# Kernel tuning notes

Measured on AMD Instinct MI355X. Metric: run time of the kernel, lower is better.

## Reference

```python
import jax, jax.numpy as jnp
import numpy as np

D_MODEL = 2048
N_HEADS = 16
HEAD_DIM = D_MODEL // N_HEADS  # 128
ROPE_THETA = 10000.0
BATCH = 2
SEQ_LEN = 2048  # == window_size -> dense causal SDPA path


def setup_inputs() -> dict:
    key = jax.random.key(0)
    ks = jax.random.split(key, 5)
    scale = 1.0 / np.sqrt(D_MODEL)
    x = jax.random.normal(ks[0], (BATCH, SEQ_LEN, D_MODEL), dtype=jnp.float32)
    # torch nn.Linear weights are stored (out_features, in_features); y = x @ W.T
    Wq = jax.random.normal(ks[1], (D_MODEL, D_MODEL), dtype=jnp.float32) * scale
    Wk = jax.random.normal(ks[2], (D_MODEL, D_MODEL), dtype=jnp.float32) * scale
    Wv = jax.random.normal(ks[3], (D_MODEL, D_MODEL), dtype=jnp.float32) * scale
    Wo = jax.random.normal(ks[4], (D_MODEL, D_MODEL), dtype=jnp.float32) * scale
    return {"x": x, "Wq": Wq, "Wk": Wk, "Wv": Wv, "Wo": Wo}


def _apply_rope(x):
    # x: [B, H, S, HEAD_DIM]; interleaved-pair RoPE, positions 0..S-1
    S = x.shape[2]
    inv_freq = 1.0 / (ROPE_THETA ** (jnp.arange(0, HEAD_DIM, 2, dtype=jnp.float32) / HEAD_DIM))
    t = jnp.arange(S, dtype=jnp.float32)
    freqs = jnp.outer(t, inv_freq)            # [S, HEAD_DIM//2]
    cos = jnp.cos(freqs)
    sin = jnp.sin(freqs)
    x1 = x[..., 0::2]
    x2 = x[..., 1::2]
    rot = jnp.stack([x1 * cos - x2 * sin, x1 * sin + x2 * cos], axis=-1)  # [B,H,S,hd/2,2]
    return rot.reshape(x.shape)


def reference(x, Wq, Wk, Wv, Wo):
    B, S, _ = x.shape
    q = (x @ Wq.T).reshape(B, S, N_HEADS, HEAD_DIM).transpose(0, 2, 1, 3)  # [B,H,S,D]
    k = (x @ Wk.T).reshape(B, S, N_HEADS, HEAD_DIM).transpose(0, 2, 1, 3)
    v = (x @ Wv.T).reshape(B, S, N_HEADS, HEAD_DIM).transpose(0, 2, 1, 3)
    q = _apply_rope(q)
    k = _apply_rope(k)
    scores = jnp.einsum("bhqd,bhkd->bhqk", q, k) / np.sqrt(HEAD_DIM).astype(np.float32)
    causal = jnp.tril(jnp.ones((S, S), dtype=bool))
    scores = jnp.where(causal, scores, -jnp.inf)
    attn = jax.nn.softmax(scores, axis=-1)
    out = jnp.einsum("bhqk,bhkd->bhqd", attn, v)
    out = out.transpose(0, 2, 1, 3).reshape(B, S, N_HEADS * HEAD_DIM)
    return out @ Wo.T
```

## Files before the change

### kernel.cpp

```cpp
#include <hip/hip_runtime.h>
#include <stdint.h>

#define D_MODEL 2048
#define SEQ     2048
#define BATCH   2
#define NHEAD   16
#define HD      128
#define MROWS   (BATCH*SEQ)

typedef short short8 __attribute__((ext_vector_type(8)));
typedef float f32x4  __attribute__((ext_vector_type(4)));

__device__ __forceinline__ unsigned short f2b(float f) {
  unsigned int u = __float_as_uint(f);
  u += 0x7fffu + ((u >> 16) & 1u);
  return (unsigned short)(u >> 16);
}
__device__ __forceinline__ float b2f(unsigned short s) {
  return __uint_as_float(((unsigned int)s) << 16);
}
__device__ __forceinline__ void gll16(const void* g, void* l) {
  __builtin_amdgcn_global_load_lds((const __attribute__((address_space(1))) void*)g,
                                   (__attribute__((address_space(3))) void*)l, 16, 0, 0);
}
__device__ __forceinline__ void barrier_nodrain() {
  asm volatile("" ::: "memory");
  __builtin_amdgcn_s_barrier();
  asm volatile("" ::: "memory");
}
template<int N> __device__ __forceinline__ void vmwait() {
  if constexpr (N == 0)       asm volatile("s_waitcnt vmcnt(0)" ::: "memory");
  else if constexpr (N == 1)  asm volatile("s_waitcnt vmcnt(1)" ::: "memory");
  else if constexpr (N == 2)  asm volatile("s_waitcnt vmcnt(2)" ::: "memory");
  else if constexpr (N == 3)  asm volatile("s_waitcnt vmcnt(3)" ::: "memory");
  else if constexpr (N == 4)  asm volatile("s_waitcnt vmcnt(4)" ::: "memory");
  else if constexpr (N == 5)  asm volatile("s_waitcnt vmcnt(5)" ::: "memory");
  else if constexpr (N == 6)  asm volatile("s_waitcnt vmcnt(6)" ::: "memory");
  else if constexpr (N == 7)  asm volatile("s_waitcnt vmcnt(7)" ::: "memory");
  else if constexpr (N == 8)  asm volatile("s_waitcnt vmcnt(8)" ::: "memory");
  else if constexpr (N == 10) asm volatile("s_waitcnt vmcnt(10)" ::: "memory");
  else                        asm volatile("s_waitcnt vmcnt(12)" ::: "memory");
}

__global__ __launch_bounds__(256) void cast_all(
    const float* __restrict__ x,  const float* __restrict__ Wq,
    const float* __restrict__ Wk, const float* __restrict__ Wv,
    const float* __restrict__ Wo, unsigned short* __restrict__ dst)
{
  size_t e = ((size_t)blockIdx.x * 256 + threadIdx.x) * 4;
  const size_t XN = (size_t)MROWS * D_MODEL;
  const size_t WN = (size_t)D_MODEL * D_MODEL;
  const float* src; size_t off;
  if (e < XN) { src = x; off = e; }
  else {
    size_t e2 = e - XN;
    int w = (int)(e2 >> 22);
    off = e2 & (WN - 1);
    src = (w == 0) ? Wq : (w == 1) ? Wk : (w == 2) ? Wv : Wo;
  }
  float4 v = *(const float4*)(src + off);
  ushort4 o;
  o.x = f2b(v.x); o.y = f2b(v.y); o.z = f2b(v.z); o.w = f2b(v.w);
  *(ushort4*)(dst + e) = o;
}

template<int BM, int LA>
__device__ __forceinline__ void gemm_2mp(
    const unsigned short* __restrict__ A, const unsigned short* __restrict__ Bw,
    unsigned short* __restrict__ As, unsigned short* __restrict__ Bs,
    int m0, int n0, int tid, f32x4 (&acc)[BM / 32][4])
{
  constexpr int K = D_MODEL, NT = K / 64;
  constexpr int HA = BM / 2;
  constexpr int MI = BM / 32, MIH = MI / 2;
  constexpr int AHALF = HA * 64;
  constexpr int BHALF = 128 * 64;
  constexpr int W1 = 2 * LA + 2;
  constexpr int W2 = 2 * LA + 4;
  const int wave = tid >> 6, lane = tid & 63, l15 = lane & 15, quad = lane >> 4;
  const int wr = wave >> 2, wc = wave & 3;
  const int rA = wr * 16 + l15;
  const int rB = wc * 16 + l15;
  const int swk = l15 & 7;

  auto stA = [&](int buf, int h, int t) {
    #pragma unroll
    for (int i = 0; i < LA; ++i) {
      int slot = i * 512 + tid, rw = slot >> 3, ch = slot & 7;
      gll16(A + (size_t)(m0 + h * HA + rw) * K + t * 64 + ((ch ^ (rw & 7)) * 8),
            As + (buf * 2 + h) * AHALF + (i * 512 + wave * 64) * 8);
    }
  };
  auto stB = [&](int buf, int h, int t) {
    #pragma unroll
    for (int i = 0; i < 2; ++i) {
      int slot = i * 512 + tid, rw = slot >> 3, ch = slot & 7;
      gll16(Bw + (size_t)(n0 + h * 128 + rw) * K + t * 64 + ((ch ^ (rw & 7)) * 8),
            Bs + (buf * 2 + h) * BHALF + (i * 512 + wave * 64) * 8);
    }
  };
  auto ldA = [&](int buf, int h, int ml, int ks) -> short8 {
    int rw = ml * 32 + rA;
    return *(const short8*)(As + (buf * 2 + h) * AHALF + rw * 64 + (((ks * 4 + quad) ^ swk) * 8));
  };
  auto ldB = [&](int buf, int h, int nl, int ks) -> short8 {
    int rw = nl * 64 + rB;
    return *(const short8*)(Bs + (buf * 2 + h) * BHALF + rw * 64 + (((ks * 4 + quad) ^ swk) * 8));
  };

  stA(0, 0, 0); stB(0, 1, 0);
  stB(0, 0, 0); stA(0, 1, 0);
  stA(1, 0, 1); stB(1, 1, 1);

  short8 ah[MIH][2], b0[2][2], b1[2][2];

  #pragma unroll 1
  for (int t = 0; t < NT; ++t) {
    const int buf = t & 1;

    if (t == NT - 1) vmwait<LA>(); else vmwait<W1>();
    barrier_nodrain();
    #pragma unroll
    for (int ml = 0; ml < MIH; ++ml) {
      ah[ml][0] = ldA(buf, 0, ml, 0); ah[ml][1] = ldA(buf, 0, ml, 1);
    }
    #pragma unroll
    for (int nl = 0; nl < 2; ++nl) {
      b0[nl][0] = ldB(buf, 0, nl, 0); b0[nl][1] = ldB(buf, 0, nl, 1);
      b1[nl][0] = ldB(buf, 1, nl, 0); b1[nl][1] = ldB(buf, 1, nl, 1);
    }
    if (t + 1 < NT) { stB(buf ^ 1, 0, t + 1); stA(buf ^ 1, 1, t + 1); }
    asm volatile("s_waitcnt lgkmcnt(0)" ::: "memory");
    __builtin_amdgcn_sched_barrier(0);
    __builtin_amdgcn_s_setprio(1);
    #pragma unroll
    for (int ml = 0; ml < MIH; ++ml)
      #pragma unroll
      for (int nl = 0; nl < 2; ++nl)
        #pragma unroll
        for (int ks = 0; ks < 2; ++ks)
          acc[ml][nl] = __builtin_amdgcn_mfma_f32_16x16x32_bf16(ah[ml][ks], b0[nl][ks], acc[ml][nl], 0, 0, 0);
    #pragma unroll
    for (int ml = 0; ml < MIH; ++ml)
      #pragma unroll
      for (int nl = 0; nl < 2; ++nl)
        #pragma unroll
        for (int ks = 0; ks < 2; ++ks)
          acc[ml][2 + nl] = __builtin_amdgcn_mfma_f32_16x16x32_bf16(ah[ml][ks], b1[nl][ks], acc[ml][2 + nl], 0, 0, 0);
    __builtin_amdgcn_s_setprio(0);

    if (t == NT - 1) vmwait<0>(); else vmwait<W2>();
    barrier_nodrain();
    #pragma unroll
    for (int ml = 0; ml < MIH; ++ml) {
      ah[ml][0] = ldA(buf, 1, ml, 0); ah[ml][1] = ldA(buf, 1, ml, 1);
    }
    if (t + 2 < NT) { stA(buf, 0, t + 2); stB(buf, 1, t + 2); }
    asm volatile("s_waitcnt lgkmcnt(0)" ::: "memory");
    __builtin_amdgcn_sched_barrier(0);
    __builtin_amdgcn_s_setprio(1);
    #pragma unroll
    for (int ml = 0; ml < MIH; ++ml)
      #pragma unroll
      for (int nl = 0; nl < 2; ++nl)
        #pragma unroll
        for (int ks = 0; ks < 2; ++ks)
          acc[MIH + ml][2 + nl] = __builtin_amdgcn_mfma_f32_16x16x32_bf16(ah[ml][ks], b1[nl][ks], acc[MIH + ml][2 + nl], 0, 0, 0);
    #pragma unroll
    for (int ml = 0; ml < MIH; ++ml)
      #pragma unroll
      for (int nl = 0; nl < 2; ++nl)
        #pragma unroll
        for (int ks = 0; ks < 2; ++ks)
          acc[MIH + ml][nl] = __builtin_amdgcn_mfma_f32_16x16x32_bf16(ah[ml][ks], b0[nl][ks], acc[MIH + ml][nl], 0, 0, 0);
    __builtin_amdgcn_s_setprio(0);
  }
}

template<int BM, int BN>
__device__ __forceinline__ void gemm_pipe(
    const unsigned short* __restrict__ A, const unsigned short* __restrict__ Bw,
    unsigned short* __restrict__ As, unsigned short* __restrict__ Bs,
    int m0, int n0, int tid, f32x4 (&acc)[BM / 32][4])
{
  constexpr int K  = D_MODEL;
  constexpr int NT = K / 64;
  constexpr int LA = BM / 64, LB = BN / 64;
  constexpr int LT = LA + LB;
  constexpr int MI = BM / 32, MH = MI / 2;
  const int wave = tid >> 6, lane = tid & 63, l15 = lane & 15, quad = lane >> 4;
  const int wr = wave >> 2, wc = wave & 3;
  const int sw = l15 & 7;
  const int arow = wr * (BM / 2) + l15;
  const int brow = wc * (BN / 4) + l15;

  auto stage = [&](int buf, int t) {
    const int kt = t * 64;
    #pragma unroll
    for (int i = 0; i < LA; ++i) {
      int slot = i * 512 + tid;
      int row = slot >> 3, ch = slot & 7;
      gll16(A + (size_t)(m0 + row) * K + kt + ((ch ^ (row & 7)) * 8),
            As + (size_t)buf * (BM * 64) + (size_t)(i * 512 + wave * 64) * 8);
    }
    #pragma unroll
    for (int i = 0; i < LB; ++i) {
      int slot = i * 512 + tid;
      int row = slot >> 3, ch = slot & 7;
      gll16(Bw + (size_t)(n0 + row) * K + kt + ((ch ^ (row & 7)) * 8),
            Bs + (size_t)buf * (BN * 64) + (size_t)(i * 512 + wave * 64) * 8);
    }
  };

  stage(0, 0);
  stage(1, 1);

  short8 ah[MH][2], bf[4][2];

  #pragma unroll 1
  for (int t = 0; t < NT; ++t) {
    const int cur = t & 1;
    if (t < NT - 1) {
      if constexpr (LT == 8) vmwait<8>(); else vmwait<6>();
    } else {
      vmwait<0>();
    }
    barrier_nodrain();

    const unsigned short* as = As + cur * (BM * 64);
    const unsigned short* bs = Bs + cur * (BN * 64);

    #pragma unroll
    for (int mi = 0; mi < MH; ++mi)
      #pragma unroll
      for (int ks = 0; ks < 2; ++ks)
        ah[mi][ks] = *(const short8*)(as + (arow + mi * 16) * 64 + (((ks * 4 + quad) ^ sw) * 8));
    #pragma unroll
    for (int ni = 0; ni < 2; ++ni)
      #pragma unroll
      for (int ks = 0; ks < 2; ++ks)
        bf[ni][ks] = *(const short8*)(bs + (brow + ni * 16) * 64 + (((ks * 4 + quad) ^ sw) * 8));
    __builtin_amdgcn_s_setprio(1);
    #pragma unroll
    for (int mi = 0; mi < MH; ++mi)
      #pragma unroll
      for (int ni = 0; ni < 2; ++ni)
        #pragma unroll
        for (int ks = 0; ks < 2; ++ks)
          acc[mi][ni] = __builtin_amdgcn_mfma_f32_16x16x32_bf16(ah[mi][ks], bf[ni][ks], acc[mi][ni], 0, 0, 0);
    __builtin_amdgcn_s_setprio(0);

    #pragma unroll
    for (int ni = 2; ni < 4; ++ni)
      #pragma unroll
      for (int ks = 0; ks < 2; ++ks)
        bf[ni][ks] = *(const short8*)(bs + (brow + ni * 16) * 64 + (((ks * 4 + quad) ^ sw) * 8));
    __builtin_amdgcn_s_setprio(1);
    #pragma unroll
    for (int mi = 0; mi < MH; ++mi)
      #pragma unroll
      for (int ni = 2; ni < 4; ++ni)
        #pragma unroll
        for (int ks = 0; ks < 2; ++ks)
          acc[mi][ni] = __builtin_amdgcn_mfma_f32_16x16x32_bf16(ah[mi][ks], bf[ni][ks], acc[mi][ni], 0, 0, 0);
    __builtin_amdgcn_s_setprio(0);

    #pragma unroll
    for (int mi = 0; mi < MH; ++mi)
      #pragma unroll
      for (int ks = 0; ks < 2; ++ks)
        ah[mi][ks] = *(const short8*)(as + (arow + (mi + MH) * 16) * 64 + (((ks * 4 + quad) ^ sw) * 8));
    __builtin_amdgcn_s_setprio(1);
    #pragma unroll
    for (int mi = 0; mi < MH; ++mi)
      #pragma unroll
      for (int ni = 2; ni < 4; ++ni)
        #pragma unroll
        for (int ks = 0; ks < 2; ++ks)
          acc[mi + MH][ni] = __builtin_amdgcn_mfma_f32_16x16x32_bf16(ah[mi][ks], bf[ni][ks], acc[mi + MH][ni], 0, 0, 0);
    #pragma unroll
    for (int mi = 0; mi < MH; ++mi)
      #pragma unroll
      for (int ni = 0; ni < 2; ++ni)
        #pragma unroll
        for (int ks = 0; ks < 2; ++ks)
          acc[mi + MH][ni] = __builtin_amdgcn_mfma_f32_16x16x32_bf16(ah[mi][ks], bf[ni][ks], acc[mi + MH][ni], 0, 0, 0);
    __builtin_amdgcn_s_setprio(0);

    barrier_nodrain();
    if (t + 2 < NT) stage(cur, t + 2);
  }
}

__global__ __launch_bounds__(512, 2) void gemm_qkv3(
    const unsigned short* __restrict__ Axb, const unsigned short* __restrict__ Wqkv,
    unsigned short* __restrict__ Qh, unsigned short* __restrict__ Kh,
    unsigned short* __restrict__ Vt)
{
  __shared__ unsigned short As[2 * 2 * 128 * 64];
  __shared__ unsigned short Bs[2 * 2 * 128 * 64];
  const int m0 = blockIdx.y * 256, n0g = blockIdx.x * 256;
  f32x4 acc[8][4];
  #pragma unroll
  for (int i = 0; i < 8; ++i)
    #pragma unroll
    for (int j = 0; j < 4; ++j) acc[i][j] = (f32x4){0.f, 0.f, 0.f, 0.f};

  gemm_2mp<256, 2>(Axb, Wqkv, As, Bs, m0, n0g, threadIdx.x, acc);

  const int tid = threadIdx.x, wave = tid >> 6, lane = tid & 63;
  const int l15 = lane & 15, quad = lane >> 4, wr = wave >> 2, wc = wave & 3;
  const int z = n0g >> 11;
  if (z < 2) {
    unsigned short* dst = z ? Kh : Qh;
    #pragma unroll
    for (int mi = 0; mi < 8; ++mi)
      #pragma unroll
      for (int ni = 0; ni < 4; ++ni) {
        int row0 = m0 + mi * 32 + wr * 16 + quad * 4;
        int col  = (n0g + ni * 64 + wc * 16 + l15) & (D_MODEL - 1);
        int h = col >> 7, d = col & (HD - 1);
        #pragma unroll
        for (int r = 0; r < 4; ++r) {
          int m = row0 + r; int bb = m >> 11; int s = m & (SEQ - 1);
          dst[((size_t)(bb * NHEAD + h) * SEQ + s) * HD + d] = f2b(acc[mi][ni][r]);
        }
      }
  } else {
    #pragma unroll
    for (int mi = 0; mi < 8; ++mi)
      #pragma unroll
      for (int ni = 0; ni < 4; ++ni) {
        int row0 = m0 + mi * 32 + wr * 16 + quad * 4;
        int col  = (n0g + ni * 64 + wc * 16 + l15) & (D_MODEL - 1);
        int h = col >> 7, d = col & (HD - 1);
        int bb = row0 >> 11; int s = row0 & (SEQ - 1);
        ushort4 pk;
        pk.x = f2b(acc[mi][ni][0]); pk.y = f2b(acc[mi][ni][1]);
        pk.z = f2b(acc[mi][ni][2]); pk.w = f2b(acc[mi][ni][3]);
        *(ushort4*)(Vt + ((size_t)(bb * NHEAD + h) * HD + d) * SEQ + s) = pk;
      }
  }
}

__global__ __launch_bounds__(512, 2) void gemm_out2(
    const unsigned short* __restrict__ A, const unsigned short* __restrict__ Wo,
    float* __restrict__ C)
{
  __shared__ unsigned short As[2 * 128 * 64];
  __shared__ unsigned short Bs[2 * 256 * 64];
  const int m0 = blockIdx.y * 128, n0 = blockIdx.x * 256;
  f32x4 acc[4][4];
  #pragma unroll
  for (int i = 0; i < 4; ++i)
    #pragma unroll
    for (int j = 0; j < 4; ++j) acc[i][j] = (f32x4){0.f, 0.f, 0.f, 0.f};

  gemm_pipe<128, 256>(A, Wo, As, Bs, m0, n0, threadIdx.x, acc);

  const int tid = threadIdx.x, wave = tid >> 6, lane = tid & 63;
  const int l15 = lane & 15, quad = lane >> 4, wr = wave >> 2, wc = wave & 3;
  #pragma unroll
  for (int mi = 0; mi < 4; ++mi)
    #pragma unroll
    for (int ni = 0; ni < 4; ++ni) {
      int row0 = m0 + wr * 64 + mi * 16 + quad * 4;
      int col  = n0 + wc * 64 + ni * 16 + l15;
      #pragma unroll
      for (int r = 0; r < 4; ++r)
        C[(size_t)(row0 + r) * D_MODEL + col] = acc[mi][ni][r];
    }
}

__global__ __launch_bounds__(256) void rope_k(unsigned short* __restrict__ Qh,
                                              unsigned short* __restrict__ Kh)
{
  unsigned short* P = blockIdx.y ? Kh : Qh;
  int rid = blockIdx.x * 4 + (threadIdx.x >> 6);
  int i = threadIdx.x & 63;
  int s = rid & (SEQ - 1);
  size_t base = (size_t)rid * HD + 2 * i;
  float inv = exp2f(-(float)i * (13.287712379549449f / 64.0f));
  float ang = (float)s * inv;
  float sn, cs; sincosf(ang, &sn, &cs);
  unsigned int pk = *(const unsigned int*)(P + base);
  float x1 = b2f((unsigned short)(pk & 0xffffu));
  float x2 = b2f((unsigned short)(pk >> 16));
  unsigned short o0 = f2b(x1 * cs - x2 * sn);
  unsigned short o1 = f2b(x1 * sn + x2 * cs);
  *(unsigned int*)(P + base) = (unsigned int)o0 | ((unsigned int)o1 << 16);
}

__global__ __launch_bounds__(256) void attn_k2(
    const unsigned short* __restrict__ Qh, const unsigned short* __restrict__ Kh,
    const unsigned short* __restrict__ Vt, unsigned short* __restrict__ Aout)
{
  __shared__ unsigned short Ks[2][64 * 128];
  __shared__ unsigned short Vs[2][128 * 64];
  __shared__ unsigned short sPb[4][16 * 72];
  const int tid = threadIdx.x;
  const int wave = tid >> 6, lane = tid & 63, l15 = lane & 15, quad = lane >> 4;
  const int bh = blockIdx.y;
  const int b = bh >> 4, h = bh & 15;
  const unsigned short* Qb = Qh + (size_t)bh * SEQ * HD;
  const unsigned short* Kb = Kh + (size_t)bh * SEQ * HD;
  const unsigned short* Vb = Vt + (size_t)bh * HD * SEQ;
  unsigned short* pw = &sPb[wave][0];
  const float scl = 0.08838834764831845f * 1.4426950408889634f;

  auto stageKV = [&](int bsel, int it) {
    const int k0 = it * 64;
    unsigned short* kd = &Ks[bsel][0];
    unsigned short* vd = &Vs[bsel][0];
    #pragma unroll
    for (int c = 0; c < 4; ++c) {
      int slot = c * 256 + tid;
      int kr = slot >> 4, pch = slot & 15;
      gll16(Kb + (size_t)(k0 + kr) * HD + ((pch ^ (kr & 15)) * 8), kd + slot * 8);
    }
    #pragma unroll
    for (int c = 0; c < 4; ++c) {
      int slot = c * 256 + tid;
      int vr = slot >> 3, pch = slot & 7;
      gll16(Vb + (size_t)vr * SEQ + k0 + ((pch ^ (vr & 7)) * 8), vd + slot * 8);
    }
  };

  #pragma unroll
  for (int half = 0; half < 2; ++half) {
    const int tile = half ? (31 - blockIdx.x) : blockIdx.x;
    const int q0w = tile * 64 + wave * 16;
    const int q = q0w + l15;

    short8 qf[4];
    #pragma unroll
    for (int c = 0; c < 4; ++c)
      qf[c] = *(const short8*)(Qb + (size_t)(q0w + l15) * HD + c * 32 + quad * 8);

    f32x4 o[8];
    #pragma unroll
    for (int dj = 0; dj < 8; ++dj) o[dj] = (f32x4){0.f, 0.f, 0.f, 0.f};
    float ms = -1e30f, ls = 0.f;

    const int trips = tile + 1;
    stageKV(0, 0);
    vmwait<0>(); barrier_nodrain();

    for (int it = 0; it < trips; ++it) {
      const int cb = it & 1;
      const int k0 = it * 64;
      if (it + 1 < trips) stageKV(cb ^ 1, it + 1);

      const unsigned short* KsB = &Ks[cb][0];
      const unsigned short* VsB = &Vs[cb][0];

      f32x4 st[4];
      #pragma unroll
      for (int ni = 0; ni < 4; ++ni) st[ni] = (f32x4){0.f, 0.f, 0.f, 0.f};
      __builtin_amdgcn_s_setprio(1);
      #pragma unroll
      for (int ni = 0; ni < 4; ++ni) {
        const int rowb = (ni * 16 + l15) * 128;
        #pragma unroll
        for (int c = 0; c < 4; ++c) {
          short8 kf = *(const short8*)(KsB + rowb + (((c * 4 + quad) ^ l15) * 8));
          st[ni] = __builtin_amdgcn_mfma_f32_16x16x32_bf16(kf, qf[c], st[ni], 0, 0, 0);
        }
      }
      __builtin_amdgcn_s_setprio(0);

      if (k0 + 63 > q0w) {
        #pragma unroll
        for (int ni = 0; ni < 4; ++ni)
          #pragma unroll
          for (int r = 0; r < 4; ++r) {
            int k = k0 + ni * 16 + quad * 4 + r;
            if (k > q) st[ni][r] = -1e30f;
          }
      }

      float lm = -1e30f;
      #pragma unroll
      for (int ni = 0; ni < 4; ++ni)
        #pragma unroll
        for (int r = 0; r < 4; ++r) lm = fmaxf(lm, st[ni][r]);
      lm = fmaxf(lm, __shfl_xor(lm, 16, 64));
      lm = fmaxf(lm, __shfl_xor(lm, 32, 64));
      float mn = fmaxf(ms, lm);
      float al = exp2f((ms - mn) * scl);
      ms = mn;
      float nm = mn * scl;
      float rs = 0.f;
      #pragma unroll
      for (int ni = 0; ni < 4; ++ni)
        #pragma unroll
        for (int r = 0; r < 4; ++r) {
          float p = exp2f(fmaf(st[ni][r], scl, -nm));
          st[ni][r] = p;
          rs += p;
        }
      rs += __shfl_xor(rs, 16, 64);
      rs += __shfl_xor(rs, 32, 64);
      ls = ls * al + rs;
      #pragma unroll
      for (int dj = 0; dj < 8; ++dj) o[dj] *= al;

      #pragma unroll
      for (int ni = 0; ni < 4; ++ni) {
        ushort4 pk;
        pk.x = f2b(st[ni][0]); pk.y = f2b(st[ni][1]);
        pk.z = f2b(st[ni][2]); pk.w = f2b(st[ni][3]);
        *(ushort4*)(pw + l15 * 72 + ni * 16 + quad * 4) = pk;
      }
      short8 pf0 = *(const short8*)(pw + l15 * 72 + quad * 8);
      short8 pf1 = *(const short8*)(pw + l15 * 72 + 32 + quad * 8);

      __builtin_amdgcn_s_setprio(1);
      #pragma unroll
      for (int dj = 0; dj < 8; ++dj) {
        const int vrow = (dj * 16 + l15) * 64;
        short8 v0 = *(const short8*)(VsB + vrow + (((quad) ^ (l15 & 7)) * 8));
        short8 v1 = *(const short8*)(VsB + vrow + (((4 + quad) ^ (l15 & 7)) * 8));
        o[dj] = __builtin_amdgcn_mfma_f32_16x16x32_bf16(v0, pf0, o[dj], 0, 0, 0);
        o[dj] = __builtin_amdgcn_mfma_f32_16x16x32_bf16(v1, pf1, o[dj], 0, 0, 0);
      }
      __builtin_amdgcn_s_setprio(0);

      vmwait<0>();
      barrier_nodrain();
    }

    float rl = 1.0f / ls;
    #pragma unroll
    for (int dj = 0; dj < 8; ++dj) {
      ushort4 pk;
      pk.x = f2b(o[dj][0] * rl); pk.y = f2b(o[dj][1] * rl);
      pk.z = f2b(o[dj][2] * rl); pk.w = f2b(o[dj][3] * rl);
      *(ushort4*)(Aout + ((size_t)(b * SEQ + q)) * D_MODEL + h * HD + dj * 16 + quad * 4) = pk;
    }
  }
}

extern "C" void kernel_launch(void* const* d_in, const int* in_sizes, int n_in,
                              void* d_out, int out_size, void* d_ws, size_t ws_size,
                              hipStream_t stream)
{
  const float* x  = (const float*)d_in[0];
  const float* Wq = (const float*)d_in[1];
  const float* Wk = (const float*)d_in[2];
  const float* Wv = (const float*)d_in[3];
  const float* Wo = (const float*)d_in[4];
  float* out = (float*)d_out;

  unsigned short* xb  = (unsigned short*)d_ws;
  unsigned short* wqb = xb  + 8388608;
  unsigned short* wkb = wqb + 4194304;
  unsigned short* wvb = wkb + 4194304;
  unsigned short* wob = wvb + 4194304;
  unsigned short* qh  = wob + 4194304;
  unsigned short* kh  = qh  + 8388608;
  unsigned short* vt  = kh  + 8388608;
  unsigned short* ao  = vt  + 8388608;

  (void)wkb; (void)wvb;
  cast_all<<<24576, 256, 0, stream>>>(x, Wq, Wk, Wv, Wo, xb);
  gemm_qkv3<<<dim3(24, 16), 512, 0, stream>>>(xb, wqb, qh, kh, vt);
  rope_k<<<dim3(16384, 2), 256, 0, stream>>>(qh, kh);
  attn_k2<<<dim3(16, 32), 256, 0, stream>>>(qh, kh, vt, ao);
  gemm_out2<<<dim3(8, 32), 512, 0, stream>>>(ao, wob, out);
}
```

Before: 391.2 us.

## Fuse RoPE into QKV GEMM epilogue and share KV tiles across paired query tiles

```diff
diff --git a/kernel.cpp b/kernel.cpp
--- a/kernel.cpp
+++ b/kernel.cpp
@@ -292,7 +292,7 @@
   }
 }
 
-__global__ __launch_bounds__(512, 2) void gemm_qkv3(
+__global__ __launch_bounds__(512, 2) void gemm_qkv4(
     const unsigned short* __restrict__ Axb, const unsigned short* __restrict__ Wqkv,
     unsigned short* __restrict__ Qh, unsigned short* __restrict__ Kh,
     unsigned short* __restrict__ Vt)
@@ -320,10 +320,17 @@
         int row0 = m0 + mi * 32 + wr * 16 + quad * 4;
         int col  = (n0g + ni * 64 + wc * 16 + l15) & (D_MODEL - 1);
         int h = col >> 7, d = col & (HD - 1);
+        int i2 = d >> 1;
+        float inv = exp2f(-(float)i2 * (13.287712379549449f / 64.0f));
+        bool ev = (d & 1) == 0;
         #pragma unroll
         for (int r = 0; r < 4; ++r) {
           int m = row0 + r; int bb = m >> 11; int s = m & (SEQ - 1);
-          dst[((size_t)(bb * NHEAD + h) * SEQ + s) * HD + d] = f2b(acc[mi][ni][r]);
+          float v  = acc[mi][ni][r];
+          float vp = __shfl_xor(v, 1, 64);
+          float sn, cs; sincosf((float)s * inv, &sn, &cs);
+          float ro = ev ? (v * cs - vp * sn) : (vp * sn + v * cs);
+          dst[((size_t)(bb * NHEAD + h) * SEQ + s) * HD + d] = f2b(ro);
         }
       }
   } else {
@@ -372,26 +379,7 @@
     }
 }
 
-__global__ __launch_bounds__(256) void rope_k(unsigned short* __restrict__ Qh,
-                                              unsigned short* __restrict__ Kh)
-{
-  unsigned short* P = blockIdx.y ? Kh : Qh;
-  int rid = blockIdx.x * 4 + (threadIdx.x >> 6);
-  int i = threadIdx.x & 63;
-  int s = rid & (SEQ - 1);
-  size_t base = (size_t)rid * HD + 2 * i;
-  float inv = exp2f(-(float)i * (13.287712379549449f / 64.0f));
-  float ang = (float)s * inv;
-  float sn, cs; sincosf(ang, &sn, &cs);
-  unsigned int pk = *(const unsigned int*)(P + base);
-  float x1 = b2f((unsigned short)(pk & 0xffffu));
-  float x2 = b2f((unsigned short)(pk >> 16));
-  unsigned short o0 = f2b(x1 * cs - x2 * sn);
-  unsigned short o1 = f2b(x1 * sn + x2 * cs);
-  *(unsigned int*)(P + base) = (unsigned int)o0 | ((unsigned int)o1 << 16);
-}
-
-__global__ __launch_bounds__(256) void attn_k2(
+__global__ __launch_bounds__(256) void attn_k3(
     const unsigned short* __restrict__ Qh, const unsigned short* __restrict__ Kh,
     const unsigned short* __restrict__ Vt, unsigned short* __restrict__ Aout)
 {
@@ -409,135 +397,147 @@
   const float scl = 0.08838834764831845f * 1.4426950408889634f;
 
   auto stageKV = [&](int bsel, int it) {
-    const int k0 = it * 64;
+    const int k0s = it * 64;
     unsigned short* kd = &Ks[bsel][0];
     unsigned short* vd = &Vs[bsel][0];
     #pragma unroll
     for (int c = 0; c < 4; ++c) {
       int slot = c * 256 + tid;
       int kr = slot >> 4, pch = slot & 15;
-      gll16(Kb + (size_t)(k0 + kr) * HD + ((pch ^ (kr & 15)) * 8), kd + slot * 8);
+      gll16(Kb + (size_t)(k0s + kr) * HD + ((pch ^ (kr & 15)) * 8), kd + slot * 8);
     }
     #pragma unroll
     for (int c = 0; c < 4; ++c) {
       int slot = c * 256 + tid;
       int vr = slot >> 3, pch = slot & 7;
-      gll16(Vb + (size_t)vr * SEQ + k0 + ((pch ^ (vr & 7)) * 8), vd + slot * 8);
-    }
-  };
-
+      gll16(Vb + (size_t)vr * SEQ + k0s + ((pch ^ (vr & 7)) * 8), vd + slot * 8);
+    }
+  };
+
+  const int tileA = blockIdx.x;
+  const int tileB = 31 - blockIdx.x;
+  const int tripsA = tileA + 1;
+  const int ntrips = tileB + 1;
+  const int q0wA = tileA * 64 + wave * 16, q0wB = tileB * 64 + wave * 16;
+  const int qA = q0wA + l15, qB = q0wB + l15;
+
+  short8 qfA[4], qfB[4];
   #pragma unroll
-  for (int half = 0; half < 2; ++half) {
-    const int tile = half ? (31 - blockIdx.x) : blockIdx.x;
-    const int q0w = tile * 64 + wave * 16;
-    const int q = q0w + l15;
-
-    short8 qf[4];
-    #pragma unroll
-    for (int c = 0; c < 4; ++c)
-      qf[c] = *(const short8*)(Qb + (size_t)(q0w + l15) * HD + c * 32 + quad * 8);
-
-    f32x4 o[8];
-    #pragma unroll
-    for (int dj = 0; dj < 8; ++dj) o[dj] = (f32x4){0.f, 0.f, 0.f, 0.f};
-    float ms = -1e30f, ls = 0.f;
-
-    const int trips = tile + 1;
-    stageKV(0, 0);
-    vmwait<0>(); barrier_nodrain();
-
-    for (int it = 0; it < trips; ++it) {
-      const int cb = it & 1;
-      const int k0 = it * 64;
-      if (it + 1 < trips) stageKV(cb ^ 1, it + 1);
-
-      const unsigned short* KsB = &Ks[cb][0];
-      const unsigned short* VsB = &Vs[cb][0];
-
-      f32x4 st[4];
-      #pragma unroll
-      for (int ni = 0; ni < 4; ++ni) st[ni] = (f32x4){0.f, 0.f, 0.f, 0.f};
-      __builtin_amdgcn_s_setprio(1);
-      #pragma unroll
-      for (int ni = 0; ni < 4; ++ni) {
-        const int rowb = (ni * 16 + l15) * 128;
-        #pragma unroll
-        for (int c = 0; c < 4; ++c) {
-          short8 kf = *(const short8*)(KsB + rowb + (((c * 4 + quad) ^ l15) * 8));
-          st[ni] = __builtin_amdgcn_mfma_f32_16x16x32_bf16(kf, qf[c], st[ni], 0, 0, 0);
+  for (int c = 0; c < 4; ++c) {
+    qfA[c] = *(const short8*)(Qb + (size_t)(q0wA + l15) * HD + c * 32 + quad * 8);
+    qfB[c] = *(const short8*)(Qb + (size_t)(q0wB + l15) * HD + c * 32 + quad * 8);
+  }
+
+  f32x4 oA[8], oB[8];
+  #pragma unroll
+  for (int dj = 0; dj < 8; ++dj) { oA[dj] = (f32x4){0.f,0.f,0.f,0.f}; oB[dj] = (f32x4){0.f,0.f,0.f,0.f}; }
+  float msA = -1e30f, lsA = 0.f, msB = -1e30f, lsB = 0.f;
+
+  stageKV(0, 0);
+  vmwait<0>(); barrier_nodrain();
+
+  auto process = [&](const short8 (&qf)[4], f32x4 (&o)[8], float& ms, float& ls,
+                     int q0w, int q, const unsigned short* KsB,
+                     const unsigned short* VsB, int k0) {
+    f32x4 st[4];
+    #pragma unroll
+    for (int ni = 0; ni < 4; ++ni) st[ni] = (f32x4){0.f, 0.f, 0.f, 0.f};
+    __builtin_amdgcn_s_setprio(1);
+    #pragma unroll
+    for (int ni = 0; ni < 4; ++ni) {
+      const int rowb = (ni * 16 + l15) * 128;
+      #pragma unroll
+      for (int c = 0; c < 4; ++c) {
+        short8 kf = *(const short8*)(KsB + rowb + (((c * 4 + quad) ^ l15) * 8));
+        st[ni] = __builtin_amdgcn_mfma_f32_16x16x32_bf16(kf, qf[c], st[ni], 0, 0, 0);
+      }
+    }
+    __builtin_amdgcn_s_setprio(0);
+
+    if (k0 + 63 > q0w) {
+      #pragma unroll
+      for (int ni = 0; ni < 4; ++ni)
+        #pragma unroll
+        for (int r = 0; r < 4; ++r) {
+          int k = k0 + ni * 16 + quad * 4 + r;
+          if (k > q) st[ni][r] = -1e30f;
         }
+    }
+
+    float lm = -1e30f;
+    #pragma unroll
+    for (int ni = 0; ni < 4; ++ni)
+      #pragma unroll
+      for (int r = 0; r < 4; ++r) lm = fmaxf(lm, st[ni][r]);
+    lm = fmaxf(lm, __shfl_xor(lm, 16, 64));
+    lm = fmaxf(lm, __shfl_xor(lm, 32, 64));
+    float mn = fmaxf(ms, lm);
+    float al = exp2f((ms - mn) * scl);
+    ms = mn;
+    float nm = mn * scl;
+    float rs = 0.f;
+    #pragma unroll
+    for (int ni = 0; ni < 4; ++ni)
+      #pragma unroll
+      for (int r = 0; r < 4; ++r) {
+        float p = exp2f(fmaf(st[ni][r], scl, -nm));
+        st[ni][r] = p;
+        rs += p;
       }
-      __builtin_amdgcn_s_setprio(0);
-
-      if (k0 + 63 > q0w) {
-        #pragma unroll
-        for (int ni = 0; ni < 4; ++ni)
-          #pragma unroll
-          for (int r = 0; r < 4; ++r) {
-            int k = k0 + ni * 16 + quad * 4 + r;
-            if (k > q) st[ni][r] = -1e30f;
-          }
-      }
-
-      float lm = -1e30f;
-      #pragma unroll
-      for (int ni = 0; ni < 4; ++ni)
-        #pragma unroll
-        for (int r = 0; r < 4; ++r) lm = fmaxf(lm, st[ni][r]);
-      lm = fmaxf(lm, __shfl_xor(lm, 16, 64));
-      lm = fmaxf(lm, __shfl_xor(lm, 32, 64));
-      float mn = fmaxf(ms, lm);
-      float al = exp2f((ms - mn) * scl);
-      ms = mn;
-      float nm = mn * scl;
-      float rs = 0.f;
-      #pragma unroll
-      for (int ni = 0; ni < 4; ++ni)
-        #pragma unroll
-        for (int r = 0; r < 4; ++r) {
-          float p = exp2f(fmaf(st[ni][r], scl, -nm));
-          st[ni][r] = p;
-          rs += p;
-        }
-      rs += __shfl_xor(rs, 16, 64);
-      rs += __shfl_xor(rs, 32, 64);
-      ls = ls * al + rs;
-      #pragma unroll
-      for (int dj = 0; dj < 8; ++dj) o[dj] *= al;
-
-      #pragma unroll
-      for (int ni = 0; ni < 4; ++ni) {
-        ushort4 pk;
-        pk.x = f2b(st[ni][0]); pk.y = f2b(st[ni][1]);
-        pk.z = f2b(st[ni][2]); pk.w = f2b(st[ni][3]);
-        *(ushort4*)(pw + l15 * 72 + ni * 16 + quad * 4) = pk;
-      }
-      short8 pf0 = *(const short8*)(pw + l15 * 72 + quad * 8);
-      short8 pf1 = *(const short8*)(pw + l15 * 72 + 32 + quad * 8);
-
-      __builtin_amdgcn_s_setprio(1);
-      #pragma unroll
-      for (int dj = 0; dj < 8; ++dj) {
-        const int vrow = (dj * 16 + l15) * 64;
-        short8 v0 = *(const short8*)(VsB + vrow + (((quad) ^ (l15 & 7)) * 8));
-        short8 v1 = *(const short8*)(VsB + vrow + (((4 + quad) ^ (l15 & 7)) * 8));
-        o[dj] = __builtin_amdgcn_mfma_f32_16x16x32_bf16(v0, pf0, o[dj], 0, 0, 0);
-        o[dj] = __builtin_amdgcn_mfma_f32_16x16x32_bf16(v1, pf1, o[dj], 0, 0, 0);
-      }
-      __builtin_amdgcn_s_setprio(0);
-
-      vmwait<0>();
-      barrier_nodrain();
-    }
-
-    float rl = 1.0f / ls;
+    rs += __shfl_xor(rs, 16, 64);
+    rs += __shfl_xor(rs, 32, 64);
+    ls = ls * al + rs;
+    #pragma unroll
+    for (int dj = 0; dj < 8; ++dj) o[dj] *= al;
+
+    #pragma unroll
+    for (int ni = 0; ni < 4; ++ni) {
+      ushort4 pk;
+      pk.x = f2b(st[ni][0]); pk.y = f2b(st[ni][1]);
+      pk.z = f2b(st[ni][2]); pk.w = f2b(st[ni][3]);
+      *(ushort4*)(pw + l15 * 72 + ni * 16 + quad * 4) = pk;
+    }
+    short8 pf0 = *(const short8*)(pw + l15 * 72 + quad * 8);
+    short8 pf1 = *(const short8*)(pw + l15 * 72 + 32 + quad * 8);
+
+    __builtin_amdgcn_s_setprio(1);
     #pragma unroll
     for (int dj = 0; dj < 8; ++dj) {
-      ushort4 pk;
-      pk.x = f2b(o[dj][0] * rl); pk.y = f2b(o[dj][1] * rl);
-      pk.z = f2b(o[dj][2] * rl); pk.w = f2b(o[dj][3] * rl);
-      *(ushort4*)(Aout + ((size_t)(b * SEQ + q)) * D_MODEL + h * HD + dj * 16 + quad * 4) = pk;
-    }
+      const int vrow = (dj * 16 + l15) * 64;
+      short8 v0 = *(const short8*)(VsB + vrow + (((quad) ^ (l15 & 7)) * 8));
+      short8 v1 = *(const short8*)(VsB + vrow + (((4 + quad) ^ (l15 & 7)) * 8));
+      o[dj] = __builtin_amdgcn_mfma_f32_16x16x32_bf16(v0, pf0, o[dj], 0, 0, 0);
+      o[dj] = __builtin_amdgcn_mfma_f32_16x16x32_bf16(v1, pf1, o[dj], 0, 0, 0);
+    }
+    __builtin_amdgcn_s_setprio(0);
+  };
+
+  for (int it = 0; it < ntrips; ++it) {
+    const int cb = it & 1;
+    const int k0 = it * 64;
+    if (it + 1 < ntrips) stageKV(cb ^ 1, it + 1);
+
+    const unsigned short* KsB = &Ks[cb][0];
+    const unsigned short* VsB = &Vs[cb][0];
+
+    if (it < tripsA)
+      process(qfA, oA, msA, lsA, q0wA, qA, KsB, VsB, k0);
+    process(qfB, oB, msB, lsB, q0wB, qB, KsB, VsB, k0);
+
+    vmwait<0>();
+    barrier_nodrain();
+  }
+
+  float rlA = 1.0f / lsA, rlB = 1.0f / lsB;
+  #pragma unroll
+  for (int dj = 0; dj < 8; ++dj) {
+    ushort4 pa, pb;
+    pa.x = f2b(oA[dj][0] * rlA); pa.y = f2b(oA[dj][1] * rlA);
+    pa.z = f2b(oA[dj][2] * rlA); pa.w = f2b(oA[dj][3] * rlA);
+    pb.x = f2b(oB[dj][0] * rlB); pb.y = f2b(oB[dj][1] * rlB);
+    pb.z = f2b(oB[dj][2] * rlB); pb.w = f2b(oB[dj][3] * rlB);
+    *(ushort4*)(Aout + ((size_t)(b * SEQ + qA)) * D_MODEL + h * HD + dj * 16 + quad * 4) = pa;
+    *(ushort4*)(Aout + ((size_t)(b * SEQ + qB)) * D_MODEL + h * HD + dj * 16 + quad * 4) = pb;
   }
 }
 
@@ -564,8 +564,7 @@
 
   (void)wkb; (void)wvb;
   cast_all<<<24576, 256, 0, stream>>>(x, Wq, Wk, Wv, Wo, xb);
-  gemm_qkv3<<<dim3(24, 16), 512, 0, stream>>>(xb, wqb, qh, kh, vt);
-  rope_k<<<dim3(16384, 2), 256, 0, stream>>>(qh, kh);
-  attn_k2<<<dim3(16, 32), 256, 0, stream>>>(qh, kh, vt, ao);
+  gemm_qkv4<<<dim3(24, 16), 512, 0, stream>>>(xb, wqb, qh, kh, vt);
+  attn_k3<<<dim3(16, 32), 256, 0, stream>>>(qh, kh, vt, ao);
   gemm_out2<<<dim3(8, 32), 512, 0, stream>>>(ao, wob, out);
 }
```

Result: slower. 489.7 us (+25.2%).
